# Performance work log

Measured on AMD Instinct MI355X. Metric: run time of the kernel, lower is better.

## Reference

```python
import jax, jax.numpy as jnp
import numpy as np
import itertools

L, F, T = 16, 2, 2**19          # levels, features/level, hashmap size
BASE, SCALE = 16, 1.5           # base resolution, per-level scale
N = 524288                      # batch of sample points
PRIMES = np.array([1, 2654435761, 805459861, 3674653429], dtype=np.uint32)


def hash_encode(x, table):
    """Multi-resolution hash-grid encoding. x: [N,d] in [0,1); table: [L,T,F]."""
    n, d = x.shape
    corners = jnp.asarray(list(itertools.product([0, 1], repeat=d)), dtype=jnp.uint32)  # [C,d]
    primes = jnp.asarray(PRIMES[:d])
    is_hi = corners.astype(bool)[None]          # [1,C,d]
    outs = []
    for l in range(L):
        res = float(np.floor(BASE * SCALE**l))
        pos = x * res
        p0f = jnp.floor(pos)
        frac = pos - p0f                         # [N,d]
        p0 = p0f.astype(jnp.uint32)
        coords = p0[:, None, :] + corners[None]  # [N,C,d] uint32 (wraps)
        m = coords * primes                      # [N,C,d]
        h = m[..., 0]
        for j in range(1, d):
            h = h ^ m[..., j]
        idx = (h % np.uint32(T)).astype(jnp.int32)              # [N,C]
        w = jnp.where(is_hi, frac[:, None, :], 1.0 - frac[:, None, :]).prod(-1)  # [N,C]
        feat = table[l][idx]                                    # [N,C,F]
        outs.append(jnp.einsum('nc,ncf->nf', w, feat))
    return jnp.concatenate(outs, axis=-1)        # [N, L*F]


def mlp(h, w_in, w_hid, w_out):
    """tcnn-style bias-free MLP, ReLU hidden, linear output."""
    h = jax.nn.relu(h @ w_in)
    for i in range(w_hid.shape[0]):
        h = jax.nn.relu(h @ w_hid[i])
    return h @ w_out


def setup_inputs() -> dict:
    key = jax.random.key(0)
    ks = jax.random.split(key, 20)
    def w(k, shape):
        fan = shape[-2]
        return jax.random.normal(k, shape, jnp.float32) / np.sqrt(fan).astype(np.float32)
    return {
        'x': jax.random.uniform(ks[0], (N, 3), jnp.float32),
        't': jax.random.uniform(ks[1], (1,), jnp.float32),
        'skip_alpha': jax.random.uniform(ks[2], (1,), jnp.float32),
        'table_s': jax.random.normal(ks[3], (L, T, F), jnp.float32) * 1e-2,
        'ws_in': w(ks[4], (32, 64)),
        'ws_hid': w(ks[5], (3, 64, 64)),
        'ws_out': w(ks[6], (64, 64)),
        'table_d': jax.random.normal(ks[7], (L, T, F), jnp.float32) * 1e-2,
        'wd_in': w(ks[8], (32, 64)),
        'wd_hid': w(ks[9], (3, 64, 64)),
        'wd_out': w(ks[10], (64, 64)),
        'w1_in': w(ks[11], (128, 64)),
        'w1_hid': w(ks[12], (1, 64, 64)),
        'w1_out': w(ks[13], (64, 128)),
        'w2_in': w(ks[14], (128, 64)),
        'w2_hid': w(ks[15], (1, 64, 64)),
        'w2_out': w(ks[16], (64, 1)),
    }


def reference(x, t, skip_alpha, table_s, ws_in, ws_hid, ws_out,
              table_d, wd_in, wd_hid, wd_out,
              w1_in, w1_hid, w1_out, w2_in, w2_hid, w2_out):
    static_features = mlp(hash_encode(x, table_s), ws_in, ws_hid, ws_out)          # [N,64]
    t_col = jnp.broadcast_to(t, (x.shape[0], 1))
    x4 = jnp.concatenate([x, t_col], axis=1)                                        # [N,4]
    dynamic_features = mlp(hash_encode(x4, table_d), wd_in, wd_hid, wd_out)        # [N,64]
    features = jnp.concatenate([static_features, dynamic_features], axis=-1)       # [N,128]
    out1 = mlp(features, w1_in, w1_hid, w1_out)                                     # [N,128]
    blended = out1 * skip_alpha + (1.0 - skip_alpha) * features
    return mlp(blended, w2_in, w2_hid, w2_out)                                      # [N,1]
```

## Files before the change

### kernel.cpp

```cpp
#include <hip/hip_runtime.h>
#include <hip/hip_bf16.h>
#include <stdint.h>

#define LVLS 16
#define TSZ  524288
#define TMASK 0x7FFFFu
#define NPTS 524288
#define P1 2654435761u
#define P2 805459861u
#define P3 3674653429u

__constant__ float RES_TAB[16] = {
    16.f, 24.f, 36.f, 54.f, 81.f, 121.f, 182.f, 273.f,
    410.f, 615.f, 922.f, 1383.f, 2075.f, 3113.f, 4670.f, 7006.f};

using f16x8 = __attribute__((ext_vector_type(8))) _Float16;
using f32x4 = __attribute__((ext_vector_type(4))) float;
using u32x8 = __attribute__((ext_vector_type(8))) uint32_t;

union PackF16 { uint32_t u; _Float16 h[2]; };

constexpr int PS = 72;

struct WPtrs { const float* p[11]; };

__global__ void k_build(const float* __restrict__ ts, const float* __restrict__ td,
                        const float* __restrict__ tptr, uint2* __restrict__ Tc,
                        WPtrs wp, _Float16* __restrict__ wdst) {
    int B = blockIdx.x;
    int tid = threadIdx.x;
    if (B < 10240) {
        int c = B & 7, j = B >> 3;
        int l, e;
        if (j < 256) {
            l = c >> 1;
            e = (c & 1) * 262144 + j * 1024 + tid * 4;
        } else if (j < 768) {
            l = 12 + (c >> 1);
            e = (j - 256) * 1024 + tid * 4;
        } else {
            l = 4 + c;
            e = (j - 768) * 1024 + tid * 4;
        }
        size_t base = (size_t)l * TSZ + (size_t)e;
        const float4* ts4 = (const float4*)ts;
        float4 s01 = ts4[base >> 1];
        float4 s23 = ts4[(base >> 1) + 1];
        float res = RES_TAB[l];
        float tv  = tptr[0];
        float pt  = tv * res;
        float fpt = floorf(pt);
        float ft  = pt - fpt;
        uint32_t ut = (uint32_t)(int)fpt;
        uint32_t h0 = (ut * P3) & TMASK;
        uint32_t h1 = ((ut + 1u) * P3) & TMASK;
        const float4* td4 = (const float4*)((const float2*)td + (size_t)l * TSZ);
        uint32_t b0 = ((uint32_t)e ^ h0) & ~3u, s0 = h0 & 3u;
        uint32_t b1 = ((uint32_t)e ^ h1) & ~3u, s1 = h1 & 3u;
        float4 A0 = td4[b0 >> 1], A1 = td4[(b0 >> 1) + 1];
        float4 B0 = td4[b1 >> 1], B1 = td4[(b1 >> 1) + 1];
        float2 a[4] = {{A0.x,A0.y},{A0.z,A0.w},{A1.x,A1.y},{A1.z,A1.w}};
        float2 b[4] = {{B0.x,B0.y},{B0.z,B0.w},{B1.x,B1.y},{B1.z,B1.w}};
        float2 sv[4] = {{s01.x,s01.y},{s01.z,s01.w},{s23.x,s23.y},{s23.z,s23.w}};
        float2 ap[4], bp[4];
        switch (s0) {
        case 0: ap[0]=a[0]; ap[1]=a[1]; ap[2]=a[2]; ap[3]=a[3]; break;
        case 1: ap[0]=a[1]; ap[1]=a[0]; ap[2]=a[3]; ap[3]=a[2]; break;
        case 2: ap[0]=a[2]; ap[1]=a[3]; ap[2]=a[0]; ap[3]=a[1]; break;
        default:ap[0]=a[3]; ap[1]=a[2]; ap[2]=a[1]; ap[3]=a[0]; break;
        }
        switch (s1) {
        case 0: bp[0]=b[0]; bp[1]=b[1]; bp[2]=b[2]; bp[3]=b[3]; break;
        case 1: bp[0]=b[1]; bp[1]=b[0]; bp[2]=b[3]; bp[3]=b[2]; break;
        case 2: bp[0]=b[2]; bp[1]=b[3]; bp[2]=b[0]; bp[3]=b[1]; break;
        default:bp[0]=b[3]; bp[1]=b[2]; bp[2]=b[1]; bp[3]=b[0]; break;
        }
        uint32_t ow[8];
#pragma unroll
        for (int jj = 0; jj < 4; jj++) {
            PackF16 o0, o1;
            o0.h[0] = (_Float16)sv[jj].x; o0.h[1] = (_Float16)sv[jj].y;
            o1.h[0] = (_Float16)((1.f - ft) * ap[jj].x + ft * bp[jj].x);
            o1.h[1] = (_Float16)((1.f - ft) * ap[jj].y + ft * bp[jj].y);
            ow[jj*2]   = o0.u;
            ow[jj*2+1] = o1.u;
        }
        uint4* dst = (uint4*)(Tc + base);
        dst[0] = make_uint4(ow[0], ow[1], ow[2], ow[3]);
        dst[1] = make_uint4(ow[4], ow[5], ow[6], ow[7]);
    } else {
        int id = (B - 10240) * 256 + tid;
        if (id >= 69632) return;
        const int OFF[16] = {0,2048,6144,10240,14336,18432,20480,24576,28672,
                             32768,36864,45056,49152,57344,65536,69632};
        const int KK[15]  = {32,64,64,64,64,32,64,64,64,64,128,64,64,128,64};
        const int NN[15]  = {64,64,64,64,64,64,64,64,64,64,64,64,128,64,64};
        const int PSEL[15]= {0,1,1,1,2,3,4,4,4,5,6,7,8,9,10};
        const int POFF[15]= {0,0,4096,8192,0,0,0,4096,8192,0,0,0,0,0,0};
        int m = 0;
        while (id >= OFF[m+1]) m++;
        int local = id - OFF[m];
        int jj   = local & 7;
        int lane = (local >> 3) & 63;
        int blk  = local >> 9;
        int KC   = KK[m] >> 5;
        int ct   = blk / KC;
        int kc   = blk - ct * KC;
        int k    = kc*32 + ((lane>>4)<<3) + jj;
        int n    = ct*16 + (lane & 15);
        const float* src = wp.p[PSEL[m]] + POFF[m];
        wdst[id] = (_Float16)src[k * NN[m] + n];
    }
}

__device__ __forceinline__ void gather1(const uint2* __restrict__ tcl,
                                        float px, float py, float pz,
                                        u32x8& va, u32x8& vb,
                                        float& wx, float& wy, float& wz) {
    float fx = floorf(px), fy = floorf(py), fz = floorf(pz);
    wx = px - fx; wy = py - fy; wz = pz - fz;
    uint32_t ux = (uint32_t)(int)fx, uy = (uint32_t)(int)fy, uz = (uint32_t)(int)fz;
    uint32_t hx0 = ux,     hx1 = ux + 1u;
    uint32_t hy0 = uy*P1,  hy1 = (uy+1u)*P1;
    uint32_t hz0 = uz*P2,  hz1 = (uz+1u)*P2;
#pragma unroll
    for (int cc = 0; cc < 8; cc++) {
        uint32_t idx = (((cc&1)?hx1:hx0) ^ ((cc&2)?hy1:hy0) ^ ((cc&4)?hz1:hz0)) & TMASK;
        uint2 t = tcl[idx];
        if (cc < 4) { va[(cc&3)*2+0] = t.x; va[(cc&3)*2+1] = t.y; }
        else        { vb[(cc&3)*2+0] = t.x; vb[(cc&3)*2+1] = t.y; }
    }
}

__device__ __forceinline__ void consume1(const u32x8& va, const u32x8& vb,
                                         float wx, float wy, float wz,
                                         uint32_t* __restrict__ es,
                                         uint32_t* __restrict__ ed, int p) {
    float wxa[2] = {1.f-wx, wx}, wya[2] = {1.f-wy, wy}, wza[2] = {1.f-wz, wz};
    float sA0 = 0.f, sA1 = 0.f, sD0 = 0.f, sD1 = 0.f;
#pragma unroll
    for (int cc = 0; cc < 8; cc++) {
        float w = wxa[cc&1] * wya[(cc>>1)&1] * wza[cc>>2];
        PackF16 s, d;
        s.u = (cc<4) ? va[(cc&3)*2+0] : vb[(cc&3)*2+0];
        d.u = (cc<4) ? va[(cc&3)*2+1] : vb[(cc&3)*2+1];
        sA0 += w*(float)s.h[0]; sA1 += w*(float)s.h[1];
        sD0 += w*(float)d.h[0]; sD1 += w*(float)d.h[1];
    }
    PackF16 o;
    o.h[0] = (_Float16)sA0; o.h[1] = (_Float16)sA1; es[p] = o.u;
    o.h[0] = (_Float16)sD0; o.h[1] = (_Float16)sD1; ed[p] = o.u;
}

#define MEMFENCE asm volatile("" ::: "memory")
#define PIN(a,b,c,d) asm volatile("" : "+v"(a), "+v"(b), "+v"(c), "+v"(d))

__launch_bounds__(256, 4)
__global__ void k_encode(const float* __restrict__ x,
                         const uint2* __restrict__ Tc,
                         uint32_t* __restrict__ EncS, uint32_t* __restrict__ EncD) {
    int tid = threadIdx.x;
    int c   = blockIdx.x & 7;
    int b   = blockIdx.x >> 3;
    int l, pb, stride;
    if (b < 256) {
        l = 4 + c;
        pb = b * 256 + tid;
        stride = 65536;
    } else if (b < 384) {
        l = 12 + (c >> 1);
        pb = (c & 1) * 262144 + (b - 256) * 256 + tid;
        stride = 32768;
    } else {
        l = c >> 1;
        pb = (c & 1) * 262144 + (b - 384) * 256 + tid;
        stride = 32768;
    }
    const uint2* tcl = Tc + (size_t)l * TSZ;
    uint32_t* es = EncS + (size_t)l * NPTS;
    uint32_t* ed = EncD + (size_t)l * NPTS;
    float res = RES_TAB[l];

    float PX[8], PY[8], PZ[8];
#pragma unroll
    for (int i = 0; i < 8; i++) {
        int p = pb + i * stride;
        PX[i] = x[p*3+0]*res; PY[i] = x[p*3+1]*res; PZ[i] = x[p*3+2]*res;
    }

    u32x8 A0, A1, A2, A3, B0, B1, B2, B3;
    float wA0x, wA0y, wA0z, wA1x, wA1y, wA1z;
    float wB0x, wB0y, wB0z, wB1x, wB1y, wB1z;

    gather1(tcl, PX[0], PY[0], PZ[0], A0, A1, wA0x, wA0y, wA0z);
    gather1(tcl, PX[1], PY[1], PZ[1], A2, A3, wA1x, wA1y, wA1z);
    gather1(tcl, PX[2], PY[2], PZ[2], B0, B1, wB0x, wB0y, wB0z);
    gather1(tcl, PX[3], PY[3], PZ[3], B2, B3, wB1x, wB1y, wB1z);
    MEMFENCE;
    PIN(A0, A1, A2, A3);
    consume1(A0, A1, wA0x, wA0y, wA0z, es, ed, pb + 0*stride);
    consume1(A2, A3, wA1x, wA1y, wA1z, es, ed, pb + 1*stride);
    gather1(tcl, PX[4], PY[4], PZ[4], A0, A1, wA0x, wA0y, wA0z);
    gather1(tcl, PX[5], PY[5], PZ[5], A2, A3, wA1x, wA1y, wA1z);
    MEMFENCE;
    PIN(B0, B1, B2, B3);
    consume1(B0, B1, wB0x, wB0y, wB0z, es, ed, pb + 2*stride);
    consume1(B2, B3, wB1x, wB1y, wB1z, es, ed, pb + 3*stride);
    gather1(tcl, PX[6], PY[6], PZ[6], B0, B1, wB0x, wB0y, wB0z);
    gather1(tcl, PX[7], PY[7], PZ[7], B2, B3, wB1x, wB1y, wB1z);
    MEMFENCE;
    PIN(A0, A1, A2, A3);
    consume1(A0, A1, wA0x, wA0y, wA0z, es, ed, pb + 4*stride);
    consume1(A2, A3, wA1x, wA1y, wA1z, es, ed, pb + 5*stride);
    PIN(B0, B1, B2, B3);
    consume1(B0, B1, wB0x, wB0y, wB0z, es, ed, pb + 6*stride);
    consume1(B2, B3, wB1x, wB1y, wB1z, es, ed, pb + 7*stride);
}

__device__ __forceinline__ void wait_lds() {
    asm volatile("s_waitcnt lgkmcnt(0)" ::: "memory");
}

template<int KC, bool RELU>
__device__ __forceinline__ void mm2(const f16x8 a[2][4], const f16x8* __restrict__ B,
                                    _Float16* dst, int m, int quad, int lane) {
#pragma unroll
    for (int ct = 0; ct < 4; ct++) {
        f32x4 acc0 = {0.f,0.f,0.f,0.f}, acc1 = {0.f,0.f,0.f,0.f};
#pragma unroll
        for (int kc = 0; kc < KC; kc++) {
            f16x8 b = B[(ct*KC+kc)*64 + lane];
            acc0 = __builtin_amdgcn_mfma_f32_16x16x32_f16(a[0][kc], b, acc0, 0, 0, 0);
            acc1 = __builtin_amdgcn_mfma_f32_16x16x32_f16(a[1][kc], b, acc1, 0, 0, 0);
        }
#pragma unroll
        for (int i = 0; i < 4; i++) {
            float v0 = acc0[i], v1 = acc1[i];
            if (RELU) { v0 = fmaxf(v0, 0.f); v1 = fmaxf(v1, 0.f); }
            dst[(0*16 + quad*4+i)*PS + ct*16 + m] = (_Float16)v0;
            dst[(1*16 + quad*4+i)*PS + ct*16 + m] = (_Float16)v1;
        }
    }
}

template<int KC>
__device__ __forceinline__ void mm2_keep(const f16x8 a[2][4], const f16x8* __restrict__ B,
                                         _Float16* dst, PackF16 P[2][8],
                                         int m, int quad, int lane) {
#pragma unroll
    for (int ct = 0; ct < 4; ct++) {
        f32x4 acc0 = {0.f,0.f,0.f,0.f}, acc1 = {0.f,0.f,0.f,0.f};
#pragma unroll
        for (int kc = 0; kc < KC; kc++) {
            f16x8 b = B[(ct*KC+kc)*64 + lane];
            acc0 = __builtin_amdgcn_mfma_f32_16x16x32_f16(a[0][kc], b, acc0, 0, 0, 0);
            acc1 = __builtin_amdgcn_mfma_f32_16x16x32_f16(a[1][kc], b, acc1, 0, 0, 0);
        }
#pragma unroll
        for (int ih = 0; ih < 2; ih++) {
            PackF16 p0, p1;
            p0.h[0] = (_Float16)acc0[ih*2+0]; p0.h[1] = (_Float16)acc0[ih*2+1];
            p1.h[0] = (_Float16)acc1[ih*2+0]; p1.h[1] = (_Float16)acc1[ih*2+1];
            P[0][ct*2+ih] = p0; P[1][ct*2+ih] = p1;
            dst[(0*16 + quad*4+ih*2+0)*PS + ct*16 + m] = p0.h[0];
            dst[(0*16 + quad*4+ih*2+1)*PS + ct*16 + m] = p0.h[1];
            dst[(1*16 + quad*4+ih*2+0)*PS + ct*16 + m] = p1.h[0];
            dst[(1*16 + quad*4+ih*2+1)*PS + ct*16 + m] = p1.h[1];
        }
    }
}

template<int KC>
__device__ __forceinline__ void read_a(const _Float16* buf, f16x8 a[2][4], int m, int quad) {
#pragma unroll
    for (int rt = 0; rt < 2; rt++)
#pragma unroll
        for (int kc = 0; kc < KC; kc++)
            a[rt][kc] = *(const f16x8*)(buf + (rt*16 + m)*PS + kc*32 + quad*8);
}

__device__ __forceinline__ void read_a128(const _Float16* Fs, const _Float16* Fd,
                                          f16x8 a[2][4], int m, int quad) {
#pragma unroll
    for (int rt = 0; rt < 2; rt++) {
#pragma unroll
        for (int kc = 0; kc < 2; kc++) {
            a[rt][kc]   = *(const f16x8*)(Fs + (rt*16 + m)*PS + kc*32 + quad*8);
            a[rt][kc+2] = *(const f16x8*)(Fd + (rt*16 + m)*PS + kc*32 + quad*8);
        }
    }
}

__device__ __forceinline__ void load_enc(const uint32_t* __restrict__ Enc,
                                         int pbase, int m, int quad, f16x8 a[2][4]) {
#pragma unroll
    for (int rt = 0; rt < 2; rt++) {
        union { uint32_t u[4]; f16x8 v; } cv;
        int p = pbase + rt*16 + m;
#pragma unroll
        for (int j = 0; j < 4; j++)
            cv.u[j] = Enc[(size_t)(quad*4 + j) * NPTS + p];
        a[rt][0] = cv.v;
    }
}

__launch_bounds__(256, 4)
__global__ void k_mlp(const uint32_t* __restrict__ EncS, const uint32_t* __restrict__ EncD,
                      const _Float16* __restrict__ Wfrag, const float* __restrict__ alphap,
                      const float* __restrict__ w2out, float* __restrict__ out) {
    __shared__ _Float16 FsB[4][32*PS];
    __shared__ _Float16 FdB[4][32*PS];
    int tid  = threadIdx.x;
    int wave = tid >> 6, lane = tid & 63;
    int m = lane & 15, quad = lane >> 4;
    int pbase = blockIdx.x * 128 + wave * 32;
    _Float16* Fs = FsB[wave];
    _Float16* Fd = FdB[wave];
    const f16x8* W8 = (const f16x8*)Wfrag;
    float alpha = alphap[0];

    f16x8 aS[2][4], aD[2][4];
    PackF16 sP[2][8], dP[2][8];

    load_enc(EncS, pbase, m, quad, aS);
    load_enc(EncD, pbase, m, quad, aD);
    mm2<1, true>(aS, W8 + 0,    Fs, m, quad, lane);
    mm2<1, true>(aD, W8 + 2304, Fd, m, quad, lane); wait_lds();
    read_a<2>(Fs, aS, m, quad); read_a<2>(Fd, aD, m, quad);
    mm2<2, true>(aS, W8 + 256,  Fs, m, quad, lane);
    mm2<2, true>(aD, W8 + 2560, Fd, m, quad, lane); wait_lds();
    read_a<2>(Fs, aS, m, quad); read_a<2>(Fd, aD, m, quad);
    mm2<2, true>(aS, W8 + 768,  Fs, m, quad, lane);
    mm2<2, true>(aD, W8 + 3072, Fd, m, quad, lane); wait_lds();
    read_a<2>(Fs, aS, m, quad); read_a<2>(Fd, aD, m, quad);
    mm2<2, true>(aS, W8 + 1280, Fs, m, quad, lane);
    mm2<2, true>(aD, W8 + 3584, Fd, m, quad, lane); wait_lds();
    read_a<2>(Fs, aS, m, quad); read_a<2>(Fd, aD, m, quad);
    mm2_keep<2>(aS, W8 + 1792, Fs, sP, m, quad, lane);
    mm2_keep<2>(aD, W8 + 4096, Fd, dP, m, quad, lane); wait_lds();
    read_a128(Fs, Fd, aS, m, quad);
    mm2<4, true>(aS, W8 + 4608, Fs, m, quad, lane); wait_lds();
    read_a<2>(Fs, aS, m, quad);
    mm2<2, true>(aS, W8 + 5632, Fs, m, quad, lane); wait_lds();
    read_a<2>(Fs, aS, m, quad);
#pragma unroll
    for (int ct = 0; ct < 8; ct++) {
        f32x4 acc0 = {0.f,0.f,0.f,0.f}, acc1 = {0.f,0.f,0.f,0.f};
#pragma unroll
        for (int kc = 0; kc < 2; kc++) {
            f16x8 b = W8[6144 + (ct*2+kc)*64 + lane];
            acc0 = __builtin_amdgcn_mfma_f32_16x16x32_f16(aS[0][kc], b, acc0, 0, 0, 0);
            acc1 = __builtin_amdgcn_mfma_f32_16x16x32_f16(aS[1][kc], b, acc1, 0, 0, 0);
        }
        _Float16* tgt = (ct < 4) ? Fs : Fd;
        int col = (ct & 3) * 16 + m;
#pragma unroll
        for (int i = 0; i < 4; i++) {
            float f0 = (ct < 4) ? (float)sP[0][ct*2 + (i>>1)].h[i&1]
                                : (float)dP[0][(ct-4)*2 + (i>>1)].h[i&1];
            float f1 = (ct < 4) ? (float)sP[1][ct*2 + (i>>1)].h[i&1]
                                : (float)dP[1][(ct-4)*2 + (i>>1)].h[i&1];
            tgt[(0*16 + quad*4+i)*PS + col] = (_Float16)(alpha*acc0[i] + (1.f-alpha)*f0);
            tgt[(1*16 + quad*4+i)*PS + col] = (_Float16)(alpha*acc1[i] + (1.f-alpha)*f1);
        }
    }
    wait_lds();
    read_a128(Fs, Fd, aS, m, quad);
    mm2<4, true>(aS, W8 + 7168, Fs, m, quad, lane); wait_lds();
    read_a<2>(Fs, aS, m, quad);
    float rsum0[4] = {0.f,0.f,0.f,0.f}, rsum1[4] = {0.f,0.f,0.f,0.f};
#pragma unroll
    for (int ct = 0; ct < 4; ct++) {
        f32x4 acc0 = {0.f,0.f,0.f,0.f}, acc1 = {0.f,0.f,0.f,0.f};
#pragma unroll
        for (int kc = 0; kc < 2; kc++) {
            f16x8 b = W8[8192 + (ct*2+kc)*64 + lane];
            acc0 = __builtin_amdgcn_mfma_f32_16x16x32_f16(aS[0][kc], b, acc0, 0, 0, 0);
            acc1 = __builtin_amdgcn_mfma_f32_16x16x32_f16(aS[1][kc], b, acc1, 0, 0, 0);
        }
        float wv = w2out[ct*16 + m];
#pragma unroll
        for (int i = 0; i < 4; i++) {
            rsum0[i] += fmaxf(acc0[i], 0.f) * wv;
            rsum1[i] += fmaxf(acc1[i], 0.f) * wv;
        }
    }
#pragma unroll
    for (int off = 1; off < 16; off <<= 1) {
#pragma unroll
        for (int i = 0; i < 4; i++) {
            rsum0[i] += __shfl_xor(rsum0[i], off, 64);
            rsum1[i] += __shfl_xor(rsum1[i], off, 64);
        }
    }
    if (m == 0) {
#pragma unroll
        for (int i = 0; i < 4; i++) {
            out[pbase + 0*16 + quad*4 + i] = rsum0[i];
            out[pbase + 1*16 + quad*4 + i] = rsum1[i];
        }
    }
}

extern "C" void kernel_launch(void* const* d_in, const int* in_sizes, int n_in,
                              void* d_out, int out_size, void* d_ws, size_t ws_size,
                              hipStream_t stream) {
    const float* x      = (const float*)d_in[0];
    const float* t      = (const float*)d_in[1];
    const float* alpha  = (const float*)d_in[2];
    const float* tab_s  = (const float*)d_in[3];
    const float* ws_in  = (const float*)d_in[4];
    const float* ws_hid = (const float*)d_in[5];
    const float* ws_out = (const float*)d_in[6];
    const float* tab_d  = (const float*)d_in[7];
    const float* wd_in  = (const float*)d_in[8];
    const float* wd_hid = (const float*)d_in[9];
    const float* wd_out = (const float*)d_in[10];
    const float* w1_in  = (const float*)d_in[11];
    const float* w1_hid = (const float*)d_in[12];
    const float* w1_out = (const float*)d_in[13];
    const float* w2_in  = (const float*)d_in[14];
    const float* w2_hid = (const float*)d_in[15];
    const float* w2_out = (const float*)d_in[16];
    float* out = (float*)d_out;

    char* ws = (char*)d_ws;
    _Float16* Wfrag = (_Float16*)ws;
    uint2*    Tc    = (uint2*)(ws + 139264);
    uint32_t* EncS  = (uint32_t*)(ws + 139264 + 67108864);
    uint32_t* EncD  = EncS + (size_t)LVLS * NPTS;
    size_t needed = 139264 + 67108864 + 2ull * 33554432ull;
    if (ws_size < needed) return;

    WPtrs wp;
    wp.p[0] = ws_in;  wp.p[1] = ws_hid; wp.p[2] = ws_out;
    wp.p[3] = wd_in;  wp.p[4] = wd_hid; wp.p[5] = wd_out;
    wp.p[6] = w1_in;  wp.p[7] = w1_hid; wp.p[8] = w1_out;
    wp.p[9] = w2_in;  wp.p[10] = w2_hid;

    k_build  <<<10512, 256, 0, stream>>>(tab_s, tab_d, t, Tc, wp, Wfrag);
    k_encode <<<4096,  256, 0, stream>>>(x, Tc, EncS, EncD);
    k_mlp    <<<NPTS/128, 256, 0, stream>>>(EncS, EncD, Wfrag, alpha, w2_out, out);
}
```

Baseline: 544.9 us.

## Keep MLP activations in registers using transposed 16x16x16 MFMA chaining

Result: slower. 595.8 us (+9.3%).

```diff
diff --git a/kernel.cpp b/kernel.cpp
--- a/kernel.cpp
+++ b/kernel.cpp
@@ -15,12 +15,11 @@
     410.f, 615.f, 922.f, 1383.f, 2075.f, 3113.f, 4670.f, 7006.f};
 
 using f16x8 = __attribute__((ext_vector_type(8))) _Float16;
+using f16x4 = __attribute__((ext_vector_type(4))) _Float16;
 using f32x4 = __attribute__((ext_vector_type(4))) float;
 using u32x8 = __attribute__((ext_vector_type(8))) uint32_t;
 
 union PackF16 { uint32_t u; _Float16 h[2]; };
-
-constexpr int PS = 72;
 
 struct WPtrs { const float* p[11]; };
 
@@ -90,26 +89,26 @@
         dst[1] = make_uint4(ow[4], ow[5], ow[6], ow[7]);
     } else {
         int id = (B - 10240) * 256 + tid;
-        if (id >= 69632) return;
-        const int OFF[16] = {0,2048,6144,10240,14336,18432,20480,24576,28672,
-                             32768,36864,45056,49152,57344,65536,69632};
-        const int KK[15]  = {32,64,64,64,64,32,64,64,64,64,128,64,64,128,64};
-        const int NN[15]  = {64,64,64,64,64,64,64,64,64,64,64,64,128,64,64};
-        const int PSEL[15]= {0,1,1,1,2,3,4,4,4,5,6,7,8,9,10};
-        const int POFF[15]= {0,0,4096,8192,0,0,0,4096,8192,0,0,0,0,0,0};
-        int m = 0;
-        while (id >= OFF[m+1]) m++;
-        int local = id - OFF[m];
-        int jj   = local & 7;
-        int lane = (local >> 3) & 63;
-        int blk  = local >> 9;
-        int KC   = KK[m] >> 5;
-        int ct   = blk / KC;
-        int kc   = blk - ct * KC;
-        int k    = kc*32 + ((lane>>4)<<3) + jj;
-        int n    = ct*16 + (lane & 15);
-        const float* src = wp.p[PSEL[m]] + POFF[m];
-        wdst[id] = (_Float16)src[k * NN[m] + n];
+        if (id >= 17408) return;
+        int lane = id & 63;
+        int t    = id >> 6;
+        const int TB[12]   = {0,8,56,72,80,128,144,176,192,224,256,272};
+        const int KCt[11]  = {2,4,4, 2,4,4, 8,4,4, 8,4};
+        const int NNt[11]  = {64,64,64, 64,64,64, 64,64,128, 64,64};
+        const int PSELt[11]= {0,1,2, 3,4,5, 6,7,8, 9,10};
+        int s = 0;
+        while (t >= TB[s+1]) s++;
+        int local = t - TB[s];
+        const float* src = wp.p[PSELt[s]];
+        if (s == 1 || s == 4) { src += (local >> 4) * 4096; local &= 15; }
+        int KC = KCt[s], N = NNt[s];
+        int ct = local / KC, kc = local - ct * KC;
+        int k0 = kc*16 + (lane >> 4)*4;
+        int n  = ct*16 + (lane & 15);
+        _Float16* d = wdst + ((size_t)t*64 + lane)*4;
+#pragma unroll
+        for (int jj = 0; jj < 4; jj++)
+            d[jj] = (_Float16)src[(k0 + jj) * N + n];
     }
 }
 
@@ -217,90 +216,47 @@
     consume1(B2, B3, wB1x, wB1y, wB1z, es, ed, pb + 7*stride);
 }
 
-__device__ __forceinline__ void wait_lds() {
-    asm volatile("s_waitcnt lgkmcnt(0)" ::: "memory");
-}
+#define MFMA16 __builtin_amdgcn_mfma_f32_16x16x16f16
 
 template<int KC, bool RELU>
-__device__ __forceinline__ void mm2(const f16x8 a[2][4], const f16x8* __restrict__ B,
-                                    _Float16* dst, int m, int quad, int lane) {
+__device__ __forceinline__ void layerx(const f16x4* __restrict__ Wt,
+                                       const f16x4 Xin[2][8], f16x4 Xout[2][8],
+                                       int lane) {
 #pragma unroll
     for (int ct = 0; ct < 4; ct++) {
         f32x4 acc0 = {0.f,0.f,0.f,0.f}, acc1 = {0.f,0.f,0.f,0.f};
 #pragma unroll
         for (int kc = 0; kc < KC; kc++) {
-            f16x8 b = B[(ct*KC+kc)*64 + lane];
-            acc0 = __builtin_amdgcn_mfma_f32_16x16x32_f16(a[0][kc], b, acc0, 0, 0, 0);
-            acc1 = __builtin_amdgcn_mfma_f32_16x16x32_f16(a[1][kc], b, acc1, 0, 0, 0);
-        }
+            f16x4 w = Wt[(ct*KC + kc)*64 + lane];
+            acc0 = MFMA16(w, Xin[0][kc], acc0, 0, 0, 0);
+            acc1 = MFMA16(w, Xin[1][kc], acc1, 0, 0, 0);
+        }
+        f16x4 o0, o1;
 #pragma unroll
         for (int i = 0; i < 4; i++) {
             float v0 = acc0[i], v1 = acc1[i];
             if (RELU) { v0 = fmaxf(v0, 0.f); v1 = fmaxf(v1, 0.f); }
-            dst[(0*16 + quad*4+i)*PS + ct*16 + m] = (_Float16)v0;
-            dst[(1*16 + quad*4+i)*PS + ct*16 + m] = (_Float16)v1;
-        }
-    }
-}
-
-template<int KC>
-__device__ __forceinline__ void mm2_keep(const f16x8 a[2][4], const f16x8* __restrict__ B,
-                                         _Float16* dst, PackF16 P[2][8],
-                                         int m, int quad, int lane) {
-#pragma unroll
-    for (int ct = 0; ct < 4; ct++) {
-        f32x4 acc0 = {0.f,0.f,0.f,0.f}, acc1 = {0.f,0.f,0.f,0.f};
-#pragma unroll
-        for (int kc = 0; kc < KC; kc++) {
-            f16x8 b = B[(ct*KC+kc)*64 + lane];
-            acc0 = __builtin_amdgcn_mfma_f32_16x16x32_f16(a[0][kc], b, acc0, 0, 0, 0);
-            acc1 = __builtin_amdgcn_mfma_f32_16x16x32_f16(a[1][kc], b, acc1, 0, 0, 0);
-        }
-#pragma unroll
-        for (int ih = 0; ih < 2; ih++) {
-            PackF16 p0, p1;
-            p0.h[0] = (_Float16)acc0[ih*2+0]; p0.h[1] = (_Float16)acc0[ih*2+1];
-            p1.h[0] = (_Float16)acc1[ih*2+0]; p1.h[1] = (_Float16)acc1[ih*2+1];
-            P[0][ct*2+ih] = p0; P[1][ct*2+ih] = p1;
-            dst[(0*16 + quad*4+ih*2+0)*PS + ct*16 + m] = p0.h[0];
-            dst[(0*16 + quad*4+ih*2+1)*PS + ct*16 + m] = p0.h[1];
-            dst[(1*16 + quad*4+ih*2+0)*PS + ct*16 + m] = p1.h[0];
-            dst[(1*16 + quad*4+ih*2+1)*PS + ct*16 + m] = p1.h[1];
-        }
-    }
-}
-
-template<int KC>
-__device__ __forceinline__ void read_a(const _Float16* buf, f16x8 a[2][4], int m, int quad) {
-#pragma unroll
-    for (int rt = 0; rt < 2; rt++)
-#pragma unroll
-        for (int kc = 0; kc < KC; kc++)
-            a[rt][kc] = *(const f16x8*)(buf + (rt*16 + m)*PS + kc*32 + quad*8);
-}
-
-__device__ __forceinline__ void read_a128(const _Float16* Fs, const _Float16* Fd,
-                                          f16x8 a[2][4], int m, int quad) {
+            o0[i] = (_Float16)v0; o1[i] = (_Float16)v1;
+        }
+        Xout[0][ct] = o0; Xout[1][ct] = o1;
+    }
+}
+
+__device__ __forceinline__ void load_enc16(const uint32_t* __restrict__ Enc,
+                                           int pbase, int m, int q,
+                                           f16x4 X[2][8]) {
 #pragma unroll
     for (int rt = 0; rt < 2; rt++) {
+        int p = pbase + rt*16 + m;
 #pragma unroll
         for (int kc = 0; kc < 2; kc++) {
-            a[rt][kc]   = *(const f16x8*)(Fs + (rt*16 + m)*PS + kc*32 + quad*8);
-            a[rt][kc+2] = *(const f16x8*)(Fd + (rt*16 + m)*PS + kc*32 + quad*8);
-        }
-    }
-}
-
-__device__ __forceinline__ void load_enc(const uint32_t* __restrict__ Enc,
-                                         int pbase, int m, int quad, f16x8 a[2][4]) {
-#pragma unroll
-    for (int rt = 0; rt < 2; rt++) {
-        union { uint32_t u[4]; f16x8 v; } cv;
-        int p = pbase + rt*16 + m;
-#pragma unroll
-        for (int j = 0; j < 4; j++)
-            cv.u[j] = Enc[(size_t)(quad*4 + j) * NPTS + p];
-        a[rt][0] = cv.v;
+            PackF16 a, b;
+            a.u = Enc[(size_t)(kc*8 + q*2 + 0) * NPTS + p];
+            b.u = Enc[(size_t)(kc*8 + q*2 + 1) * NPTS + p];
+            f16x4 v;
+            v[0] = a.h[0]; v[1] = a.h[1]; v[2] = b.h[0]; v[3] = b.h[1];
+            X[rt][kc] = v;
+        }
     }
 }
 
@@ -308,97 +264,109 @@
 __global__ void k_mlp(const uint32_t* __restrict__ EncS, const uint32_t* __restrict__ EncD,
                       const _Float16* __restrict__ Wfrag, const float* __restrict__ alphap,
                       const float* __restrict__ w2out, float* __restrict__ out) {
-    __shared__ _Float16 FsB[4][32*PS];
-    __shared__ _Float16 FdB[4][32*PS];
     int tid  = threadIdx.x;
     int wave = tid >> 6, lane = tid & 63;
-    int m = lane & 15, quad = lane >> 4;
+    int m = lane & 15, q = lane >> 4;
     int pbase = blockIdx.x * 128 + wave * 32;
-    _Float16* Fs = FsB[wave];
-    _Float16* Fd = FdB[wave];
-    const f16x8* W8 = (const f16x8*)Wfrag;
+    const f16x4* W4 = (const f16x4*)Wfrag;
     float alpha = alphap[0];
 
-    f16x8 aS[2][4], aD[2][4];
-    PackF16 sP[2][8], dP[2][8];
-
-    load_enc(EncS, pbase, m, quad, aS);
-    load_enc(EncD, pbase, m, quad, aD);
-    mm2<1, true>(aS, W8 + 0,    Fs, m, quad, lane);
-    mm2<1, true>(aD, W8 + 2304, Fd, m, quad, lane); wait_lds();
-    read_a<2>(Fs, aS, m, quad); read_a<2>(Fd, aD, m, quad);
-    mm2<2, true>(aS, W8 + 256,  Fs, m, quad, lane);
-    mm2<2, true>(aD, W8 + 2560, Fd, m, quad, lane); wait_lds();
-    read_a<2>(Fs, aS, m, quad); read_a<2>(Fd, aD, m, quad);
-    mm2<2, true>(aS, W8 + 768,  Fs, m, quad, lane);
-    mm2<2, true>(aD, W8 + 3072, Fd, m, quad, lane); wait_lds();
-    read_a<2>(Fs, aS, m, quad); read_a<2>(Fd, aD, m, quad);
-    mm2<2, true>(aS, W8 + 1280, Fs, m, quad, lane);
-    mm2<2, true>(aD, W8 + 3584, Fd, m, quad, lane); wait_lds();
-    read_a<2>(Fs, aS, m, quad); read_a<2>(Fd, aD, m, quad);
-    mm2_keep<2>(aS, W8 + 1792, Fs, sP, m, quad, lane);
-    mm2_keep<2>(aD, W8 + 4096, Fd, dP, m, quad, lane); wait_lds();
-    read_a128(Fs, Fd, aS, m, quad);
-    mm2<4, true>(aS, W8 + 4608, Fs, m, quad, lane); wait_lds();
-    read_a<2>(Fs, aS, m, quad);
-    mm2<2, true>(aS, W8 + 5632, Fs, m, quad, lane); wait_lds();
-    read_a<2>(Fs, aS, m, quad);
-#pragma unroll
-    for (int ct = 0; ct < 8; ct++) {
-        f32x4 acc0 = {0.f,0.f,0.f,0.f}, acc1 = {0.f,0.f,0.f,0.f};
-#pragma unroll
-        for (int kc = 0; kc < 2; kc++) {
-            f16x8 b = W8[6144 + (ct*2+kc)*64 + lane];
-            acc0 = __builtin_amdgcn_mfma_f32_16x16x32_f16(aS[0][kc], b, acc0, 0, 0, 0);
-            acc1 = __builtin_amdgcn_mfma_f32_16x16x32_f16(aS[1][kc], b, acc1, 0, 0, 0);
-        }
-        _Float16* tgt = (ct < 4) ? Fs : Fd;
-        int col = (ct & 3) * 16 + m;
-#pragma unroll
-        for (int i = 0; i < 4; i++) {
-            float f0 = (ct < 4) ? (float)sP[0][ct*2 + (i>>1)].h[i&1]
-                                : (float)dP[0][(ct-4)*2 + (i>>1)].h[i&1];
-            float f1 = (ct < 4) ? (float)sP[1][ct*2 + (i>>1)].h[i&1]
-                                : (float)dP[1][(ct-4)*2 + (i>>1)].h[i&1];
-            tgt[(0*16 + quad*4+i)*PS + col] = (_Float16)(alpha*acc0[i] + (1.f-alpha)*f0);
-            tgt[(1*16 + quad*4+i)*PS + col] = (_Float16)(alpha*acc1[i] + (1.f-alpha)*f1);
-        }
-    }
-    wait_lds();
-    read_a128(Fs, Fd, aS, m, quad);
-    mm2<4, true>(aS, W8 + 7168, Fs, m, quad, lane); wait_lds();
-    read_a<2>(Fs, aS, m, quad);
-    float rsum0[4] = {0.f,0.f,0.f,0.f}, rsum1[4] = {0.f,0.f,0.f,0.f};
+    f16x4 T1[2][8], T2[2][8], Ys[2][8], Yd[2][8];
+
+    load_enc16(EncD, pbase, m, q, T1);
+    layerx<2, true >(W4 +  72*64, T1, T2, lane);
+    layerx<4, true >(W4 +  80*64, T2, T1, lane);
+    layerx<4, true >(W4 +  96*64, T1, T2, lane);
+    layerx<4, true >(W4 + 112*64, T2, T1, lane);
+    layerx<4, false>(W4 + 128*64, T1, Yd, lane);
+    load_enc16(EncS, pbase, m, q, T1);
+    layerx<2, true >(W4 +   0*64, T1, T2, lane);
+    layerx<4, true >(W4 +   8*64, T2, T1, lane);
+    layerx<4, true >(W4 +  24*64, T1, T2, lane);
+    layerx<4, true >(W4 +  40*64, T2, T1, lane);
+    layerx<4, false>(W4 +  56*64, T1, Ys, lane);
 #pragma unroll
     for (int ct = 0; ct < 4; ct++) {
         f32x4 acc0 = {0.f,0.f,0.f,0.f}, acc1 = {0.f,0.f,0.f,0.f};
 #pragma unroll
-        for (int kc = 0; kc < 2; kc++) {
-            f16x8 b = W8[8192 + (ct*2+kc)*64 + lane];
-            acc0 = __builtin_amdgcn_mfma_f32_16x16x32_f16(aS[0][kc], b, acc0, 0, 0, 0);
-            acc1 = __builtin_amdgcn_mfma_f32_16x16x32_f16(aS[1][kc], b, acc1, 0, 0, 0);
-        }
-        float wv = w2out[ct*16 + m];
+        for (int kc = 0; kc < 8; kc++) {
+            f16x4 w  = W4[(144 + ct*8 + kc)*64 + lane];
+            f16x4 x0 = (kc < 4) ? Ys[0][kc] : Yd[0][kc-4];
+            f16x4 x1 = (kc < 4) ? Ys[1][kc] : Yd[1][kc-4];
+            acc0 = MFMA16(w, x0, acc0, 0, 0, 0);
+            acc1 = MFMA16(w, x1, acc1, 0, 0, 0);
+        }
+        f16x4 o0, o1;
 #pragma unroll
         for (int i = 0; i < 4; i++) {
-            rsum0[i] += fmaxf(acc0[i], 0.f) * wv;
-            rsum1[i] += fmaxf(acc1[i], 0.f) * wv;
-        }
-    }
-#pragma unroll
-    for (int off = 1; off < 16; off <<= 1) {
+            o0[i] = (_Float16)fmaxf(acc0[i], 0.f);
+            o1[i] = (_Float16)fmaxf(acc1[i], 0.f);
+        }
+        T1[0][ct] = o0; T1[1][ct] = o1;
+    }
+    layerx<4, true>(W4 + 176*64, T1, T2, lane);
+#pragma unroll
+    for (int h2 = 0; h2 < 2; h2++) {
+#pragma unroll
+        for (int ct = 0; ct < 4; ct++) {
+            f32x4 acc0 = {0.f,0.f,0.f,0.f}, acc1 = {0.f,0.f,0.f,0.f};
+#pragma unroll
+            for (int kc = 0; kc < 4; kc++) {
+                f16x4 w = W4[(192 + (h2*4+ct)*4 + kc)*64 + lane];
+                acc0 = MFMA16(w, T2[0][kc], acc0, 0, 0, 0);
+                acc1 = MFMA16(w, T2[1][kc], acc1, 0, 0, 0);
+            }
+            f16x4 s0 = h2 ? Yd[0][ct] : Ys[0][ct];
+            f16x4 s1 = h2 ? Yd[1][ct] : Ys[1][ct];
+            f16x4 o0, o1;
+#pragma unroll
+            for (int i = 0; i < 4; i++) {
+                o0[i] = (_Float16)(alpha*acc0[i] + (1.f-alpha)*(float)s0[i]);
+                o1[i] = (_Float16)(alpha*acc1[i] + (1.f-alpha)*(float)s1[i]);
+            }
+            T1[0][h2*4+ct] = o0; T1[1][h2*4+ct] = o1;
+        }
+    }
+#pragma unroll
+    for (int ct = 0; ct < 4; ct++) {
+        f32x4 acc0 = {0.f,0.f,0.f,0.f}, acc1 = {0.f,0.f,0.f,0.f};
+#pragma unroll
+        for (int kc = 0; kc < 8; kc++) {
+            f16x4 w = W4[(224 + ct*8 + kc)*64 + lane];
+            acc0 = MFMA16(w, T1[0][kc], acc0, 0, 0, 0);
+            acc1 = MFMA16(w, T1[1][kc], acc1, 0, 0, 0);
+        }
+        f16x4 o0, o1;
 #pragma unroll
         for (int i = 0; i < 4; i++) {
-            rsum0[i] += __shfl_xor(rsum0[i], off, 64);
-            rsum1[i] += __shfl_xor(rsum1[i], off, 64);
-        }
-    }
-    if (m == 0) {
+            o0[i] = (_Float16)fmaxf(acc0[i], 0.f);
+            o1[i] = (_Float16)fmaxf(acc1[i], 0.f);
+        }
+        T2[0][ct] = o0; T2[1][ct] = o1;
+    }
+    float rs0 = 0.f, rs1 = 0.f;
+#pragma unroll
+    for (int ct = 0; ct < 4; ct++) {
+        f32x4 acc0 = {0.f,0.f,0.f,0.f}, acc1 = {0.f,0.f,0.f,0.f};
+#pragma unroll
+        for (int kc = 0; kc < 4; kc++) {
+            f16x4 w = W4[(256 + ct*4 + kc)*64 + lane];
+            acc0 = MFMA16(w, T2[0][kc], acc0, 0, 0, 0);
+            acc1 = MFMA16(w, T2[1][kc], acc1, 0, 0, 0);
+        }
+        float4 wv = *(const float4*)(w2out + ct*16 + q*4);
+        const float* wvp = (const float*)&wv;
 #pragma unroll
         for (int i = 0; i < 4; i++) {
-            out[pbase + 0*16 + quad*4 + i] = rsum0[i];
-            out[pbase + 1*16 + quad*4 + i] = rsum1[i];
-        }
+            rs0 += fmaxf(acc0[i], 0.f) * wvp[i];
+            rs1 += fmaxf(acc1[i], 0.f) * wvp[i];
+        }
+    }
+    rs0 += __shfl_xor(rs0, 16, 64); rs0 += __shfl_xor(rs0, 32, 64);
+    rs1 += __shfl_xor(rs1, 16, 64); rs1 += __shfl_xor(rs1, 32, 64);
+    if (q == 0) {
+        out[pbase +  0 + m] = rs0;
+        out[pbase + 16 + m] = rs1;
     }
 }
 
@@ -438,7 +406,7 @@
     wp.p[6] = w1_in;  wp.p[7] = w1_hid; wp.p[8] = w1_out;
     wp.p[9] = w2_in;  wp.p[10] = w2_hid;
 
-    k_build  <<<10512, 256, 0, stream>>>(tab_s, tab_d, t, Tc, wp, Wfrag);
+    k_build  <<<10308, 256, 0, stream>>>(tab_s, tab_d, t, Tc, wp, Wfrag);
     k_encode <<<4096,  256, 0, stream>>>(x, Tc, EncS, EncD);
     k_mlp    <<<NPTS/128, 256, 0, stream>>>(EncS, EncD, Wfrag, alpha, w2_out, out);
 }
```
